# Performance work log

Measured on AMD Instinct MI355X. Metric: run time of the kernel, lower is better.

The kernel has to match this reference:

```python
import jax, jax.numpy as jnp
import numpy as np

S, B, I, H, O = 512, 256, 64, 512, 25

def setup_inputs() -> dict:
    key = jax.random.key(0)
    ks = jax.random.split(key, 7)
    k = 1.0 / np.sqrt(H)  # torch nn.RNN / nn.Linear default init bound
    x = jax.random.normal(ks[0], (S, B, I), dtype=jnp.float32)
    W_ih = jax.random.uniform(ks[1], (H, I), jnp.float32, -k, k)
    W_hh = jax.random.uniform(ks[2], (H, H), jnp.float32, -k, k)
    b_ih = jax.random.uniform(ks[3], (H,), jnp.float32, -k, k)
    b_hh = jax.random.uniform(ks[4], (H,), jnp.float32, -k, k)
    W2 = jax.random.uniform(ks[5], (O, H), jnp.float32, -k, k)
    b2 = jax.random.uniform(ks[6], (O,), jnp.float32, -k, k)
    return {"x": x, "W_ih": W_ih, "W_hh": W_hh, "b_ih": b_ih, "b_hh": b_hh, "W2": W2, "b2": b2}

def reference(x, W_ih, W_hh, b_ih, b_hh, W2, b2):
    # Precompute input projection for all timesteps in one big GEMM: (S,B,H)
    xi = jnp.einsum('sbi,hi->sbh', x, W_ih) + b_ih
    h0 = jnp.zeros((x.shape[1], W_hh.shape[0]), dtype=x.dtype)
    W_hh_T = W_hh.T
    def step(h_prev, xi_t):
        h = jax.nn.relu(xi_t + h_prev @ W_hh_T + b_hh)
        return h, h
    _, out = jax.lax.scan(step, h0, xi)  # out: (S, B, H)
    # Faithful to original: out[:, -1, :] selects last batch element -> (S, H)
    y = out[:, -1, :] @ W2.T + b2  # (S, 25)
    return y
```

## Files before the change

kernel.cpp:

```cpp
#include <hip/hip_runtime.h>


#define S_ 512
#define B_ 256
#define I_ 64
#define H_ 512
#define O_ 25
#define G_ 16
#define R_ 32

static __device__ __forceinline__ void wg_barrier_lds() {
  __builtin_amdgcn_sched_barrier(0);
  asm volatile("s_waitcnt lgkmcnt(0)" ::: "memory");
  __builtin_amdgcn_s_barrier();
  __builtin_amdgcn_sched_barrier(0);
}

__global__ __launch_bounds__(256) void rnn_pre(
    const float* __restrict__ x, const float* __restrict__ W_ih,
    const float* __restrict__ b_ih, const float* __restrict__ b_hh,
    float* __restrict__ xh, unsigned* __restrict__ hg) {
  const int t = blockIdx.x;
  const int tid = threadIdx.x;
  const int o = blockIdx.y * 256 + tid;
  if (t == 0 && blockIdx.y == 0) {
    hg[tid] = 0x80000000u;
    hg[tid + 256] = 0x80000000u;
    hg[tid + 512] = 0x80000000u;
    hg[tid + 768] = 0x80000000u;
  }
  __shared__ float xr[I_];
  if (tid < I_) xr[tid] = x[(t * B_ + (B_ - 1)) * I_ + tid];
  __syncthreads();
  float acc = b_ih[o] + b_hh[o];
  const float4* wp = (const float4*)(W_ih + o * I_);
#pragma unroll
  for (int j = 0; j < I_ / 4; ++j) {
    float4 w4 = wp[j];
    acc += w4.x * xr[4 * j] + w4.y * xr[4 * j + 1] + w4.z * xr[4 * j + 2] +
           w4.w * xr[4 * j + 3];
  }
  xh[t * H_ + o] = acc;
}

__global__ __launch_bounds__(256) void rnn_seq(
    const float* __restrict__ W_hh, float* __restrict__ xh,
    unsigned* hg) {
  const int tid = threadIdx.x;
  const int b = blockIdx.x;
  const int r = tid & 31;
  const int seg = tid >> 5;
  const int row = b * R_ + r;
  const int k0 = seg * 64;
  const int wave = tid >> 6;
  const int own_lo = b * R_;

  __shared__ __align__(16) float h_l[H_];
  __shared__ __align__(16) float part[R_ * 4];

  float w[64];
  {
    const float4* wp = (const float4*)(W_hh + row * H_ + k0);
#pragma unroll
    for (int j = 0; j < 16; ++j) {
      float4 v = wp[j];
      w[4 * j] = v.x; w[4 * j + 1] = v.y;
      w[4 * j + 2] = v.z; w[4 * j + 3] = v.w;
    }
  }
  for (int n = tid; n < H_; n += 256) h_l[n] = 0.0f;

  float xiv = (tid < R_) ? xh[own_lo + tid] : 0.0f;
  wg_barrier_lds();

  const bool ownp = (tid >= b * (R_ / 2)) && (tid < (b + 1) * (R_ / 2));
  const unsigned long long sm = 0x8000000080000000ull;
  int D = 0;

  for (int s = 0; s < S_; ++s) {
    float a0 = 0.f, a1 = 0.f, a2 = 0.f, a3 = 0.f;
    const float4* hp = (const float4*)(h_l + k0);
#pragma unroll
    for (int j = 0; j < 16; ++j) {
      float4 hv = hp[j];
      a0 = fmaf(w[4 * j + 0], hv.x, a0);
      a1 = fmaf(w[4 * j + 1], hv.y, a1);
      a2 = fmaf(w[4 * j + 2], hv.z, a2);
      a3 = fmaf(w[4 * j + 3], hv.w, a3);
    }
    float acc = (a0 + a1) + (a2 + a3);
    acc += __shfl_xor(acc, 32, 64);
    if ((tid & 32) == 0) part[r * 4 + wave] = acc;
    wg_barrier_lds();

    const unsigned phase = (unsigned)((s >> 1) & 1);
    unsigned* buf = hg + (s & 1) * H_;

    if (tid < R_) {
      float4 p4 = *(const float4*)(part + tid * 4);
      float sum = p4.x + p4.y + p4.z + p4.w + xiv;
      float h = fmaxf(sum, 0.0f);
      __hip_atomic_store(&buf[own_lo + tid],
                         __float_as_uint(h) | (phase << 31),
                         __ATOMIC_RELAXED, __HIP_MEMORY_SCOPE_AGENT);
      h_l[own_lo + tid] = h;
      xh[s * H_ + own_lo + tid] = h;
    }

    if (s == S_ - 1) break;

    if (tid < R_) xiv = xh[(s + 1) * H_ + own_lo + tid];

    if (!ownp) {
      for (int d = 0; d < D; ++d) __builtin_amdgcn_s_sleep(1);
      const unsigned long long ph64 = phase ? sm : 0ull;
      const unsigned long long* ap = (const unsigned long long*)buf + tid;
      unsigned long long v;
      int n = 0;
      do {
        v = __hip_atomic_load(ap, __ATOMIC_RELAXED, __HIP_MEMORY_SCOPE_AGENT);
        ++n;
      } while (((v ^ ph64) & sm) != 0ull);
      float2 hv;
      hv.x = __uint_as_float((unsigned)v & 0x7fffffffu);
      hv.y = __uint_as_float((unsigned)(v >> 32) & 0x7fffffffu);
      *(float2*)(h_l + 2 * tid) = hv;
      if (n > 1) {
        D += (n - 1);
        if (D > 40) D = 40;
      } else if ((s & 7) == 0 && D > 0) {
        --D;
      }
    }
    wg_barrier_lds();
  }
}

__global__ __launch_bounds__(256) void rnn_post(
    const float* __restrict__ hseq, const float* __restrict__ W2,
    const float* __restrict__ b2, float* __restrict__ y) {
  const int t = blockIdx.x;
  const int tid = threadIdx.x;
  __shared__ float hl[H_];
  __shared__ float part[256];
  for (int n = tid; n < H_; n += 256) hl[n] = hseq[t * H_ + n];
  __syncthreads();
  const int o = tid >> 3;
  const int seg = tid & 7;
  float acc = 0.0f;
  if (o < O_) {
    const float4* wp = (const float4*)(W2 + o * H_ + seg * 64);
    const float4* hp = (const float4*)(hl + seg * 64);
#pragma unroll
    for (int j = 0; j < 16; ++j) {
      float4 w4 = wp[j];
      float4 h4 = hp[j];
      acc += w4.x * h4.x + w4.y * h4.y + w4.z * h4.z + w4.w * h4.w;
    }
  }
  part[tid] = acc;
  __syncthreads();
  if (tid < O_) {
    float sum = 0.0f;
#pragma unroll
    for (int j = 0; j < 8; ++j) sum += part[tid * 8 + j];
    y[t * O_ + tid] = sum + b2[tid];
  }
}

extern "C" void kernel_launch(void* const* d_in, const int* in_sizes, int n_in,
                              void* d_out, int out_size, void* d_ws, size_t ws_size,
                              hipStream_t stream) {
  const float* x    = (const float*)d_in[0];
  const float* W_ih = (const float*)d_in[1];
  const float* W_hh = (const float*)d_in[2];
  const float* b_ih = (const float*)d_in[3];
  const float* b_hh = (const float*)d_in[4];
  const float* W2   = (const float*)d_in[5];
  const float* b2   = (const float*)d_in[6];
  float* y = (float*)d_out;

  float* xh = (float*)d_ws;
  unsigned* hg = (unsigned*)(xh + S_ * H_);

  rnn_pre<<<dim3(S_, 2), 256, 0, stream>>>(x, W_ih, b_ih, b_hh, xh, hg);
  rnn_seq<<<G_, 256, 0, stream>>>(W_hh, xh, hg);
  rnn_post<<<S_, 256, 0, stream>>>(xh, W2, b2, y);
}
```

Measured before the change: 753.3 us.

## Keep hidden state in registers, polling global flags per thread without LDS barrier

Each thread now loads its own 64-element slice of the hidden state straight from the global phase-tagged buffer into registers and spins until every phase bit matches. This removes the shared h_l array and the second workgroup barrier per step. The partial-sum LDS buffer is double-buffered so the single remaining barrier is enough. It adds redundant global polling (every thread reads 32 qwords, 8 copies of each slice per block), uses fabs to strip the phase bit, switches the store to an atomic exchange, and enlarges the backoff, which may raise L2 traffic and register pressure.

Result: slower. 1.485 ms (+97.1%).

```diff
diff --git a/kernel.cpp b/kernel.cpp
--- a/kernel.cpp
+++ b/kernel.cpp
@@ -43,7 +43,7 @@
   xh[t * H_ + o] = acc;
 }
 
-__global__ __launch_bounds__(256) void rnn_seq(
+__global__ __launch_bounds__(256, 1) void rnn_seq(
     const float* __restrict__ W_hh, float* __restrict__ xh,
     unsigned* hg) {
   const int tid = threadIdx.x;
@@ -55,8 +55,7 @@
   const int wave = tid >> 6;
   const int own_lo = b * R_;
 
-  __shared__ __align__(16) float h_l[H_];
-  __shared__ __align__(16) float part[R_ * 4];
+  __shared__ __align__(16) float part[2][R_ * 4];
 
   float w[64];
   {
@@ -68,42 +67,46 @@
       w[4 * j + 2] = v.z; w[4 * j + 3] = v.w;
     }
   }
-  for (int n = tid; n < H_; n += 256) h_l[n] = 0.0f;
+
+  unsigned long long hv[32];
+#pragma unroll
+  for (int j = 0; j < 32; ++j) hv[j] = 0ull;
 
   float xiv = (tid < R_) ? xh[own_lo + tid] : 0.0f;
-  wg_barrier_lds();
-
-  const bool ownp = (tid >= b * (R_ / 2)) && (tid < (b + 1) * (R_ / 2));
+
   const unsigned long long sm = 0x8000000080000000ull;
   int D = 0;
 
   for (int s = 0; s < S_; ++s) {
+    const int ps = s & 1;
     float a0 = 0.f, a1 = 0.f, a2 = 0.f, a3 = 0.f;
-    const float4* hp = (const float4*)(h_l + k0);
 #pragma unroll
     for (int j = 0; j < 16; ++j) {
-      float4 hv = hp[j];
-      a0 = fmaf(w[4 * j + 0], hv.x, a0);
-      a1 = fmaf(w[4 * j + 1], hv.y, a1);
-      a2 = fmaf(w[4 * j + 2], hv.z, a2);
-      a3 = fmaf(w[4 * j + 3], hv.w, a3);
+      unsigned long long q0 = hv[2 * j], q1 = hv[2 * j + 1];
+      float h0 = __uint_as_float((unsigned)q0);
+      float h1 = __uint_as_float((unsigned)(q0 >> 32));
+      float h2 = __uint_as_float((unsigned)q1);
+      float h3 = __uint_as_float((unsigned)(q1 >> 32));
+      a0 = fmaf(w[4 * j + 0], __builtin_fabsf(h0), a0);
+      a1 = fmaf(w[4 * j + 1], __builtin_fabsf(h1), a1);
+      a2 = fmaf(w[4 * j + 2], __builtin_fabsf(h2), a2);
+      a3 = fmaf(w[4 * j + 3], __builtin_fabsf(h3), a3);
     }
     float acc = (a0 + a1) + (a2 + a3);
     acc += __shfl_xor(acc, 32, 64);
-    if ((tid & 32) == 0) part[r * 4 + wave] = acc;
+    if ((tid & 32) == 0) part[ps][r * 4 + wave] = acc;
     wg_barrier_lds();
 
     const unsigned phase = (unsigned)((s >> 1) & 1);
-    unsigned* buf = hg + (s & 1) * H_;
+    unsigned* buf = hg + ps * H_;
 
     if (tid < R_) {
-      float4 p4 = *(const float4*)(part + tid * 4);
+      float4 p4 = *(const float4*)(&part[ps][tid * 4]);
       float sum = p4.x + p4.y + p4.z + p4.w + xiv;
       float h = fmaxf(sum, 0.0f);
-      __hip_atomic_store(&buf[own_lo + tid],
-                         __float_as_uint(h) | (phase << 31),
-                         __ATOMIC_RELAXED, __HIP_MEMORY_SCOPE_AGENT);
-      h_l[own_lo + tid] = h;
+      (void)__hip_atomic_exchange(&buf[own_lo + tid],
+                                  __float_as_uint(h) | (phase << 31),
+                                  __ATOMIC_RELAXED, __HIP_MEMORY_SCOPE_AGENT);
       xh[s * H_ + own_lo + tid] = h;
     }
 
@@ -111,28 +114,40 @@
 
     if (tid < R_) xiv = xh[(s + 1) * H_ + own_lo + tid];
 
-    if (!ownp) {
-      for (int d = 0; d < D; ++d) __builtin_amdgcn_s_sleep(1);
-      const unsigned long long ph64 = phase ? sm : 0ull;
-      const unsigned long long* ap = (const unsigned long long*)buf + tid;
-      unsigned long long v;
-      int n = 0;
-      do {
-        v = __hip_atomic_load(ap, __ATOMIC_RELAXED, __HIP_MEMORY_SCOPE_AGENT);
-        ++n;
-      } while (((v ^ ph64) & sm) != 0ull);
-      float2 hv;
-      hv.x = __uint_as_float((unsigned)v & 0x7fffffffu);
-      hv.y = __uint_as_float((unsigned)(v >> 32) & 0x7fffffffu);
-      *(float2*)(h_l + 2 * tid) = hv;
-      if (n > 1) {
-        D += (n - 1);
-        if (D > 40) D = 40;
-      } else if ((s & 7) == 0 && D > 0) {
-        --D;
+    for (int d = 0; d < D; ++d) __builtin_amdgcn_s_sleep(1);
+    const unsigned long long* ap = (const unsigned long long*)buf + seg * 32;
+    int n = 0;
+    for (;;) {
+      ++n;
+#pragma unroll
+      for (int j = 0; j < 32; ++j)
+        hv[j] = __hip_atomic_load(ap + j, __ATOMIC_RELAXED,
+                                  __HIP_MEMORY_SCOPE_AGENT);
+      unsigned long long m0, m1, m2, m3;
+      if (phase) {
+        m0 = hv[0]; m1 = hv[1]; m2 = hv[2]; m3 = hv[3];
+#pragma unroll
+        for (int j = 1; j < 8; ++j) {
+          m0 &= hv[4 * j + 0]; m1 &= hv[4 * j + 1];
+          m2 &= hv[4 * j + 2]; m3 &= hv[4 * j + 3];
+        }
+        if ((~(m0 & m1 & m2 & m3) & sm) == 0ull) break;
+      } else {
+        m0 = hv[0]; m1 = hv[1]; m2 = hv[2]; m3 = hv[3];
+#pragma unroll
+        for (int j = 1; j < 8; ++j) {
+          m0 |= hv[4 * j + 0]; m1 |= hv[4 * j + 1];
+          m2 |= hv[4 * j + 2]; m3 |= hv[4 * j + 3];
+        }
+        if (((m0 | m1 | m2 | m3) & sm) == 0ull) break;
       }
     }
-    wg_barrier_lds();
+    if (n > 1) {
+      D += 8 * (n - 1);
+      if (D > 48) D = 48;
+    } else if ((s & 7) == 0 && D > 0) {
+      --D;
+    }
   }
 }
 
```

## Add step-tagged sc0 exchange path, double-buffered LDS, and spread workgroups across XCDs

Applied to the files above, without the earlier changes.

Launches 128 blocks and keeps only every eighth one, so the 16 active workgroups presumably land on different chiplets or CUs. Each producer now writes a 64-bit {value, step} record with sc0 stores, and consumers poll it with sc0 dwordx4 loads for a few tries before falling back to the old phase-bit spin path. The in-block reduction switches from an LDS partial-sum array plus a barrier to xor-shuffles within 8-lane groups. h is double-buffered in padded LDS, which removes one workgroup barrier per step. The risks are the extra global traffic, reliance on sc0 cache-coherence behaviour, and a sticky fallback heuristic when the fast path keeps missing.

Result: slower. 1.523 ms (+102.2%).

```diff
diff --git a/kernel.cpp b/kernel.cpp
--- a/kernel.cpp
+++ b/kernel.cpp
@@ -8,6 +8,11 @@
 #define O_ 25
 #define G_ 16
 #define R_ 32
+#define NC_ 128
+#define PAD_ 68
+#define PADI(i) ((((i) >> 6) * PAD_) + ((i) & 63))
+
+typedef unsigned u32x4 __attribute__((ext_vector_type(4)));
 
 static __device__ __forceinline__ void wg_barrier_lds() {
   __builtin_amdgcn_sched_barrier(0);
@@ -28,6 +33,11 @@
     hg[tid + 256] = 0x80000000u;
     hg[tid + 512] = 0x80000000u;
     hg[tid + 768] = 0x80000000u;
+    unsigned long long* sc = (unsigned long long*)(hg + 2 * H_);
+    sc[tid] = 0xFFFFFFFF00000000ull;
+    sc[tid + 256] = 0xFFFFFFFF00000000ull;
+    sc[tid + 512] = 0xFFFFFFFF00000000ull;
+    sc[tid + 768] = 0xFFFFFFFF00000000ull;
   }
   __shared__ float xr[I_];
   if (tid < I_) xr[tid] = x[(t * B_ + (B_ - 1)) * I_ + tid];
@@ -46,21 +56,22 @@
 __global__ __launch_bounds__(256) void rnn_seq(
     const float* __restrict__ W_hh, float* __restrict__ xh,
     unsigned* hg) {
+  if (blockIdx.x & 7) return;
+  const int b = blockIdx.x >> 3;
   const int tid = threadIdx.x;
-  const int b = blockIdx.x;
-  const int r = tid & 31;
-  const int seg = tid >> 5;
-  const int row = b * R_ + r;
-  const int k0 = seg * 64;
-  const int wave = tid >> 6;
+  const int kc = tid & 7;
+  const int rloc = ((tid >> 6) << 3) | ((tid >> 3) & 7);
   const int own_lo = b * R_;
-
-  __shared__ __align__(16) float h_l[H_];
-  __shared__ __align__(16) float part[R_ * 4];
+  const bool prod = (tid & 7) == 0;
+  const int grow = own_lo + rloc;
+
+  unsigned long long* sc = (unsigned long long*)(hg + 2 * H_);
+
+  __shared__ __align__(16) float hbuf[2][8 * PAD_];
 
   float w[64];
   {
-    const float4* wp = (const float4*)(W_hh + row * H_ + k0);
+    const float4* wp = (const float4*)(W_hh + (own_lo + rloc) * H_ + kc * 64);
 #pragma unroll
     for (int j = 0; j < 16; ++j) {
       float4 v = wp[j];
@@ -68,18 +79,21 @@
       w[4 * j + 2] = v.z; w[4 * j + 3] = v.w;
     }
   }
-  for (int n = tid; n < H_; n += 256) h_l[n] = 0.0f;
-
-  float xiv = (tid < R_) ? xh[own_lo + tid] : 0.0f;
-  wg_barrier_lds();
+  for (int n = tid; n < 2 * 8 * PAD_; n += 256) ((float*)hbuf)[n] = 0.0f;
+
+  float xiv = prod ? xh[grow] : 0.0f;
 
   const bool ownp = (tid >= b * (R_ / 2)) && (tid < (b + 1) * (R_ / 2));
   const unsigned long long sm = 0x8000000080000000ull;
   int D = 0;
+  int miss = 0;
+  bool scOn = true;
+  wg_barrier_lds();
 
   for (int s = 0; s < S_; ++s) {
+    const int ps = s & 1;
     float a0 = 0.f, a1 = 0.f, a2 = 0.f, a3 = 0.f;
-    const float4* hp = (const float4*)(h_l + k0);
+    const float4* hp = (const float4*)(&hbuf[ps][kc * PAD_]);
 #pragma unroll
     for (int j = 0; j < 16; ++j) {
       float4 hv = hp[j];
@@ -89,48 +103,75 @@
       a3 = fmaf(w[4 * j + 3], hv.w, a3);
     }
     float acc = (a0 + a1) + (a2 + a3);
-    acc += __shfl_xor(acc, 32, 64);
-    if ((tid & 32) == 0) part[r * 4 + wave] = acc;
-    wg_barrier_lds();
+    acc += __shfl_xor(acc, 1);
+    acc += __shfl_xor(acc, 2);
+    acc += __shfl_xor(acc, 4);
 
     const unsigned phase = (unsigned)((s >> 1) & 1);
-    unsigned* buf = hg + (s & 1) * H_;
-
-    if (tid < R_) {
-      float4 p4 = *(const float4*)(part + tid * 4);
-      float sum = p4.x + p4.y + p4.z + p4.w + xiv;
-      float h = fmaxf(sum, 0.0f);
-      __hip_atomic_store(&buf[own_lo + tid],
-                         __float_as_uint(h) | (phase << 31),
+    unsigned* buf = hg + ps * H_;
+    unsigned long long* scb = sc + ps * H_;
+
+    if (prod) {
+      float h = fmaxf(acc + xiv, 0.0f);
+      unsigned hb = __float_as_uint(h);
+      unsigned long long sv =
+          ((unsigned long long)(unsigned)s << 32) | (unsigned long long)hb;
+      unsigned long long* sp = scb + grow;
+      asm volatile("global_store_dwordx2 %0, %1, off sc0"
+                   :: "v"(sp), "v"(sv) : "memory");
+      __hip_atomic_store(&buf[grow], hb | (phase << 31),
                          __ATOMIC_RELAXED, __HIP_MEMORY_SCOPE_AGENT);
-      h_l[own_lo + tid] = h;
-      xh[s * H_ + own_lo + tid] = h;
+      hbuf[ps ^ 1][PADI(grow)] = h;
+      xh[s * H_ + grow] = h;
     }
 
     if (s == S_ - 1) break;
 
-    if (tid < R_) xiv = xh[(s + 1) * H_ + own_lo + tid];
+    if (prod) xiv = xh[(s + 1) * H_ + grow];
 
     if (!ownp) {
-      for (int d = 0; d < D; ++d) __builtin_amdgcn_s_sleep(1);
-      const unsigned long long ph64 = phase ? sm : 0ull;
-      const unsigned long long* ap = (const unsigned long long*)buf + tid;
-      unsigned long long v;
-      int n = 0;
-      do {
-        v = __hip_atomic_load(ap, __ATOMIC_RELAXED, __HIP_MEMORY_SCOPE_AGENT);
-        ++n;
-      } while (((v ^ ph64) & sm) != 0ull);
-      float2 hv;
-      hv.x = __uint_as_float((unsigned)v & 0x7fffffffu);
-      hv.y = __uint_as_float((unsigned)(v >> 32) & 0x7fffffffu);
-      *(float2*)(h_l + 2 * tid) = hv;
-      if (n > 1) {
-        D += (n - 1);
-        if (D > 40) D = 40;
-      } else if ((s & 7) == 0 && D > 0) {
-        --D;
+      bool got = false;
+      float2 hv2;
+      if (scOn) {
+        const u32x4* sp4 = (const u32x4*)scb + tid;
+        for (int it = 0; it < 6; ++it) {
+          u32x4 v;
+          asm volatile(
+              "global_load_dwordx4 %0, %1, off sc0\n\ts_waitcnt vmcnt(0)"
+              : "=v"(v) : "v"(sp4) : "memory");
+          if (v.y == (unsigned)s && v.w == (unsigned)s) {
+            hv2.x = __uint_as_float(v.x);
+            hv2.y = __uint_as_float(v.z);
+            got = true;
+            break;
+          }
+        }
+        if (s >= 8) {
+          if (got) miss = 0;
+          else if (++miss >= 4) scOn = false;
+        }
       }
+      if (!got) {
+        for (int d = 0; d < D; ++d) __builtin_amdgcn_s_sleep(1);
+        const unsigned long long ph64 = phase ? sm : 0ull;
+        const unsigned long long* ap = (const unsigned long long*)buf + tid;
+        unsigned long long v;
+        int n = 0;
+        do {
+          v = __hip_atomic_load(ap, __ATOMIC_RELAXED,
+                                __HIP_MEMORY_SCOPE_AGENT);
+          ++n;
+        } while (((v ^ ph64) & sm) != 0ull);
+        hv2.x = __uint_as_float((unsigned)v & 0x7fffffffu);
+        hv2.y = __uint_as_float((unsigned)(v >> 32) & 0x7fffffffu);
+        if (n > 1) {
+          D += 8 * (n - 1);
+          if (D > 48) D = 48;
+        } else if ((s & 7) == 0 && D > 0) {
+          --D;
+        }
+      }
+      *(float2*)(&hbuf[ps ^ 1][PADI(2 * tid)]) = hv2;
     }
     wg_barrier_lds();
   }
@@ -184,6 +225,6 @@
   unsigned* hg = (unsigned*)(xh + S_ * H_);
 
   rnn_pre<<<dim3(S_, 2), 256, 0, stream>>>(x, W_ih, b_ih, b_hh, xh, hg);
-  rnn_seq<<<G_, 256, 0, stream>>>(W_hh, xh, hg);
+  rnn_seq<<<NC_, 256, 0, stream>>>(W_hh, xh, hg);
   rnn_post<<<S_, 256, 0, stream>>>(xh, W2, b2, y);
 }
```

## Remove mid-step barrier via in-wave row reduction and double-buffered padded h

Applied to the files above, without the earlier changes.

Each wave now owns eight complete W_hh rows, with eight lanes per row, so the row dot product is reduced by wave shuffles rather than through an LDS partial buffer. This removes one workgroup barrier per timestep. The hidden state lives in a double-buffered LDS array padded to 68 floats per 64-element chunk to reduce bank conflicts, and each step writes the next buffer. The spin-wait backoff is retuned to a larger initial sleep, faster growth, a higher cap and slower decay, which may add latency if it overshoots.

Result: slower. 1.721 ms (+128.5%).

```diff
diff --git a/kernel.cpp b/kernel.cpp
--- a/kernel.cpp
+++ b/kernel.cpp
@@ -8,6 +8,8 @@
 #define O_ 25
 #define G_ 16
 #define R_ 32
+#define PAD_ 68
+#define PADI(i) ((((i) >> 6) * PAD_) + ((i) & 63))
 
 static __device__ __forceinline__ void wg_barrier_lds() {
   __builtin_amdgcn_sched_barrier(0);
@@ -48,68 +50,69 @@
     unsigned* hg) {
   const int tid = threadIdx.x;
   const int b = blockIdx.x;
-  const int r = tid & 31;
-  const int seg = tid >> 5;
-  const int row = b * R_ + r;
-  const int k0 = seg * 64;
-  const int wave = tid >> 6;
+  const int w = tid >> 6;
+  const int l = tid & 63;
+  const int rr = l >> 3;
+  const int kc = l & 7;
   const int own_lo = b * R_;
+  const int rloc = w * 8 + rr;
+  const int grow = own_lo + rloc;
+  const bool prod = (l < 8);
+  const int prow = own_lo + w * 8 + l;
 
-  __shared__ __align__(16) float h_l[H_];
-  __shared__ __align__(16) float part[R_ * 4];
+  __shared__ __align__(16) float hbuf[2][8 * PAD_];
 
-  float w[64];
+  float wr[64];
   {
-    const float4* wp = (const float4*)(W_hh + row * H_ + k0);
+    const float4* wp = (const float4*)(W_hh + grow * H_ + kc * 64);
 #pragma unroll
     for (int j = 0; j < 16; ++j) {
       float4 v = wp[j];
-      w[4 * j] = v.x; w[4 * j + 1] = v.y;
-      w[4 * j + 2] = v.z; w[4 * j + 3] = v.w;
+      wr[4 * j] = v.x; wr[4 * j + 1] = v.y;
+      wr[4 * j + 2] = v.z; wr[4 * j + 3] = v.w;
     }
   }
-  for (int n = tid; n < H_; n += 256) h_l[n] = 0.0f;
+  for (int n = tid; n < 2 * 8 * PAD_; n += 256) ((float*)hbuf)[n] = 0.0f;
 
-  float xiv = (tid < R_) ? xh[own_lo + tid] : 0.0f;
-  wg_barrier_lds();
+  float xiv = prod ? xh[prow] : 0.0f;
 
   const bool ownp = (tid >= b * (R_ / 2)) && (tid < (b + 1) * (R_ / 2));
   const unsigned long long sm = 0x8000000080000000ull;
-  int D = 0;
+  int D = 16;
+  wg_barrier_lds();
 
   for (int s = 0; s < S_; ++s) {
+    const int ps = s & 1;
     float a0 = 0.f, a1 = 0.f, a2 = 0.f, a3 = 0.f;
-    const float4* hp = (const float4*)(h_l + k0);
+    const float4* hp = (const float4*)(&hbuf[ps][kc * PAD_]);
 #pragma unroll
     for (int j = 0; j < 16; ++j) {
       float4 hv = hp[j];
-      a0 = fmaf(w[4 * j + 0], hv.x, a0);
-      a1 = fmaf(w[4 * j + 1], hv.y, a1);
-      a2 = fmaf(w[4 * j + 2], hv.z, a2);
-      a3 = fmaf(w[4 * j + 3], hv.w, a3);
+      a0 = fmaf(wr[4 * j + 0], hv.x, a0);
+      a1 = fmaf(wr[4 * j + 1], hv.y, a1);
+      a2 = fmaf(wr[4 * j + 2], hv.z, a2);
+      a3 = fmaf(wr[4 * j + 3], hv.w, a3);
     }
     float acc = (a0 + a1) + (a2 + a3);
-    acc += __shfl_xor(acc, 32, 64);
-    if ((tid & 32) == 0) part[r * 4 + wave] = acc;
-    wg_barrier_lds();
+    acc += __shfl_xor(acc, 1);
+    acc += __shfl_xor(acc, 2);
+    acc += __shfl_xor(acc, 4);
+    float rsum = __shfl(acc, 8 * (l & 7), 64);
 
     const unsigned phase = (unsigned)((s >> 1) & 1);
-    unsigned* buf = hg + (s & 1) * H_;
+    unsigned* buf = hg + ps * H_;
 
-    if (tid < R_) {
-      float4 p4 = *(const float4*)(part + tid * 4);
-      float sum = p4.x + p4.y + p4.z + p4.w + xiv;
-      float h = fmaxf(sum, 0.0f);
-      __hip_atomic_store(&buf[own_lo + tid],
-                         __float_as_uint(h) | (phase << 31),
+    if (prod) {
+      float h = fmaxf(rsum + xiv, 0.0f);
+      __hip_atomic_store(&buf[prow], __float_as_uint(h) | (phase << 31),
                          __ATOMIC_RELAXED, __HIP_MEMORY_SCOPE_AGENT);
-      h_l[own_lo + tid] = h;
-      xh[s * H_ + own_lo + tid] = h;
+      hbuf[ps ^ 1][PADI(prow)] = h;
+      xh[s * H_ + prow] = h;
     }
 
     if (s == S_ - 1) break;
 
-    if (tid < R_) xiv = xh[(s + 1) * H_ + own_lo + tid];
+    if (prod) xiv = xh[(s + 1) * H_ + prow];
 
     if (!ownp) {
       for (int d = 0; d < D; ++d) __builtin_amdgcn_s_sleep(1);
@@ -124,11 +127,11 @@
       float2 hv;
       hv.x = __uint_as_float((unsigned)v & 0x7fffffffu);
       hv.y = __uint_as_float((unsigned)(v >> 32) & 0x7fffffffu);
-      *(float2*)(h_l + 2 * tid) = hv;
+      *(float2*)(&hbuf[ps ^ 1][PADI(2 * tid)]) = hv;
       if (n > 1) {
-        D += (n - 1);
-        if (D > 40) D = 40;
-      } else if ((s & 7) == 0 && D > 0) {
+        D += 4 * (n - 1);
+        if (D > 56) D = 56;
+      } else if ((s & 15) == 0 && D > 0) {
         --D;
       }
     }
```
